# Performance work log

Hardware: AMD Instinct MI355X
Metric: run time of the kernel (lower is better)

Reference implementation:

```python
import jax, jax.numpy as jnp
import numpy as np

N = 200000      # nodes
E = 1600000     # directed edges (before self-loops)
G = 5000        # graphs (molecules)
IN, HID, OUT, HEADS = 128, 128, 128, 3


def gat_layer(x, src, dst, W, a_src, a_dst, b, heads, out_dim, concat):
    n = x.shape[0]
    h = (x @ W).reshape(n, heads, out_dim)                 # [N,H,F]
    al_s = jnp.einsum('nhf,hf->nh', h, a_src)              # [N,H]
    al_d = jnp.einsum('nhf,hf->nh', h, a_dst)
    e = jax.nn.leaky_relu(al_s[src] + al_d[dst], 0.2)      # [E,H]
    m = jax.ops.segment_max(e, dst, num_segments=n)        # softmax over incoming edges
    ex = jnp.exp(e - m[dst])
    den = jax.ops.segment_sum(ex, dst, num_segments=n)
    alpha = ex / (den[dst] + 1e-16)                        # [E,H]
    msg = h[src] * alpha[..., None]                        # [E,H,F]
    agg = jax.ops.segment_sum(msg, dst, num_segments=n)    # [N,H,F]
    agg = agg.reshape(n, heads * out_dim) if concat else agg.mean(axis=1)
    return agg + b


def setup_inputs() -> dict:
    key = jax.random.key(0)
    ks = jax.random.split(key, 16)
    d = {}
    d['x'] = jax.random.normal(ks[0], (N, IN), dtype=jnp.float32)
    d['edge_index'] = jax.random.randint(ks[1], (2, E), 0, N, dtype=jnp.int64)
    d['batch'] = jnp.sort(jax.random.randint(ks[2], (N,), 0, G, dtype=jnp.int64))
    s = 0.1
    d['W1'] = jax.random.normal(ks[3], (IN, HEADS * HID), jnp.float32) * s
    d['a1s'] = jax.random.normal(ks[4], (HEADS, HID), jnp.float32) * s
    d['a1d'] = jax.random.normal(ks[5], (HEADS, HID), jnp.float32) * s
    d['b1'] = jnp.zeros((HEADS * HID,), jnp.float32)
    d['W2'] = jax.random.normal(ks[6], (HEADS * HID, HEADS * HID), jnp.float32) * s
    d['a2s'] = jax.random.normal(ks[7], (HEADS, HID), jnp.float32) * s
    d['a2d'] = jax.random.normal(ks[8], (HEADS, HID), jnp.float32) * s
    d['b2'] = jnp.zeros((HEADS * HID,), jnp.float32)
    d['W3'] = jax.random.normal(ks[9], (HEADS * HID, OUT), jnp.float32) * s
    d['a3s'] = jax.random.normal(ks[10], (1, OUT), jnp.float32) * s
    d['a3d'] = jax.random.normal(ks[11], (1, OUT), jnp.float32) * s
    d['b3'] = jnp.zeros((OUT,), jnp.float32)
    return d


def reference(x, edge_index, batch, W1, a1s, a1d, b1, W2, a2s, a2d, b2, W3, a3s, a3d, b3):
    # PyG GATConv default add_self_loops=True
    loops = jnp.arange(N, dtype=edge_index.dtype)
    src = jnp.concatenate([edge_index[0], loops])
    dst = jnp.concatenate([edge_index[1], loops])
    h = jax.nn.leaky_relu(gat_layer(x, src, dst, W1, a1s, a1d, b1, HEADS, HID, True), 0.2)
    h = jax.nn.leaky_relu(gat_layer(h, src, dst, W2, a2s, a2d, b2, HEADS, HID, True), 0.2)
    h = jax.nn.leaky_relu(gat_layer(h, src, dst, W3, a3s, a3d, b3, 1, OUT, False), 0.2)
    # global mean pool over graphs
    sums = jax.ops.segment_sum(h, batch, num_segments=G)            # [G,OUT]
    cnt = jax.ops.segment_sum(jnp.ones((N,), h.dtype), batch, num_segments=G)
    return sums / jnp.maximum(cnt, 1.0)[:, None]
```

## Files before the change

### kernel.cpp

```cpp
#include <hip/hip_runtime.h>
#include <hip/hip_bf16.h>
#include <math.h>

#define LRELU_SLOPE 0.2f
typedef __hip_bfloat16 bf16;
typedef __hip_bfloat162 bf16x2;

typedef short s8v __attribute__((ext_vector_type(8)));
typedef short s4v __attribute__((ext_vector_type(4)));
typedef float f4v __attribute__((ext_vector_type(4)));
typedef int   i4v __attribute__((ext_vector_type(4)));
typedef unsigned int u4v __attribute__((ext_vector_type(4)));

__device__ __forceinline__ float lrelu(float v) { return v > 0.f ? v : LRELU_SLOPE * v; }
__device__ __forceinline__ float b2f(short b) {
  return __uint_as_float(((unsigned)(unsigned short)b) << 16);
}

__device__ __forceinline__ void st2(float* p, float x, float y) {
  *(float2*)p = float2{x, y};
}

__device__ __forceinline__ u4v make_srd(const void* p) {
  u4v r;
  unsigned long long a = (unsigned long long)p;
  r.x = (unsigned)a; r.y = (unsigned)(a >> 32);
  r.z = 0xFFFFFFFFu;
  r.w = 0x00020000u;
  return r;
}
__device__ __forceinline__ void bstore16_nt(u4v srd, int byteoff, i4v d) {
  asm volatile("buffer_store_dwordx4 %0, %1, %2, 0 offen sc1 nt"
               :: "v"(d), "v"(byteoff), "s"(srd));
}


__global__ void k_zero(unsigned int* __restrict__ p, long n) {
  long i = (long)blockIdx.x * blockDim.x + threadIdx.x;
  if (i < n) p[i] = 0u;
}

__global__ void k_zero_out(float* __restrict__ out, int n) {
  int i = blockIdx.x * blockDim.x + threadIdx.x;
  if (i < n) out[i] = 0.f;
}


__global__ void k_cvt(const float* __restrict__ x, bf16* __restrict__ xb, long n) {
  long i = (long)blockIdx.x * blockDim.x + threadIdx.x;
  if (i < n) xb[i] = __float2bfloat16(x[i]);
}

__global__ void k_tw2(const float* __restrict__ W, bf16* __restrict__ B2, int K, int NN) {
  int tid = blockIdx.x * blockDim.x + threadIdx.x;
  int total = (K * NN) >> 3;
  if (tid >= total) return;
  int f = tid >> 6, l = tid & 63;
  int nfr = NN >> 4;
  int k32 = f / nfr, bnG = f - k32 * nfr;
  int col = bnG * 16 + (l & 15);
  int krow = k32 * 32 + (l >> 4) * 8;
  s8v v;
#pragma unroll
  for (int j = 0; j < 8; ++j) {
    bf16 b = __float2bfloat16(W[(size_t)(krow + j) * NN + col]);
    v[j] = *(short*)&b;
  }
  *(s8v*)&B2[(size_t)tid * 8] = v;
}


__global__ void k_hist(const int* __restrict__ dst, int* __restrict__ deg, int E, int Et) {
  int e = blockIdx.x * blockDim.x + threadIdx.x;
  if (e >= Et) return;
  int d = (e < E) ? dst[e] : (e - E);
  atomicAdd(&deg[d], 1);
}

__global__ void k_hist1(const int* __restrict__ idx, int* __restrict__ deg, int n) {
  int i = blockIdx.x * blockDim.x + threadIdx.x;
  if (i < n) atomicAdd(&deg[idx[i]], 1);
}

__global__ void k_scan1(const int* __restrict__ deg, int* __restrict__ offs,
                        int* __restrict__ bsum, int n) {
  __shared__ int sd[256];
  int t = threadIdx.x;
  int base = blockIdx.x * 1024 + t * 4;
  int v[4]; int tsum = 0;
#pragma unroll
  for (int i = 0; i < 4; ++i) { v[i] = (base + i < n) ? deg[base + i] : 0; tsum += v[i]; }
  sd[t] = tsum;
  __syncthreads();
  for (int off = 1; off < 256; off <<= 1) {
    int x = (t >= off) ? sd[t - off] : 0;
    __syncthreads();
    sd[t] += x;
    __syncthreads();
  }
  int excl = sd[t] - tsum;
#pragma unroll
  for (int i = 0; i < 4; ++i) { if (base + i < n) offs[base + i] = excl; excl += v[i]; }
  if (t == 255) bsum[blockIdx.x] = sd[255];
}

__global__ void k_scan2(int* bsum, int nb) {
  int t = threadIdx.x;
  if (nb > 256) {
    if (t == 0 && blockIdx.x == 0) {
      int run = 0;
      for (int i = 0; i < nb; ++i) { int x = bsum[i]; bsum[i] = run; run += x; }
    }
    return;
  }
  int v = (t < nb) ? bsum[t] : 0;
  int lane = t & 63, wv = t >> 6;
  int s = v;
#pragma unroll
  for (int off = 1; off < 64; off <<= 1) {
    int u = __shfl_up(s, off, 64);
    if (lane >= off) s += u;
  }
  __shared__ int wsum[4];
  if (lane == 63) wsum[wv] = s;
  __syncthreads();
  int add = 0;
  for (int w = 0; w < wv; ++w) add += wsum[w];
  if (t < nb) bsum[t] = add + s - v;
}

__global__ void k_scan3(int* __restrict__ offs, const int* __restrict__ bsum, int n, int total) {
  int t = threadIdx.x;
  int base = blockIdx.x * 1024 + t * 4;
  int add = bsum[blockIdx.x];
#pragma unroll
  for (int i = 0; i < 4; ++i) if (base + i < n) offs[base + i] += add;
  if (blockIdx.x == 0 && t == 0) offs[n] = total;
}

__global__ void k_scatter(const int* __restrict__ src, const int* __restrict__ dst,
                          const int* __restrict__ offs, int* __restrict__ cur,
                          int* __restrict__ ssrc, int E, int Et) {
  int e = blockIdx.x * blockDim.x + threadIdx.x;
  if (e >= Et) return;
  int s, d;
  if (e < E) { s = src[e]; d = dst[e]; } else { s = d = e - E; }
  int pos = offs[d] + atomicAdd(&cur[d], 1);
  ssrc[pos] = s;
}


template <int NT, int K, int NN>
__global__ __launch_bounds__(512) void k_gemm_d(const bf16* __restrict__ A,
                                                const bf16* __restrict__ B2,
                                                bf16* __restrict__ C) {
  constexpr int nk = K >> 5;
  int t = threadIdx.x;
  int wv = t >> 6, lane = t & 63;
  int mg = wv >> 2, ng = wv & 3;
  int quad = lane >> 4, l15 = lane & 15;
  size_t bm0 = (size_t)blockIdx.x * 64;
  const bf16* Ap0 = A + (bm0 + mg * 32 + l15) * (size_t)K + quad * 8;
  const bf16* Ap1 = Ap0 + (size_t)16 * K;
  constexpr int nfr = NN >> 4;
  const bf16* Bp = B2 + ((size_t)(ng * NT) << 9) + lane * 8;
  constexpr size_t fstep = (size_t)nfr << 9;

  f4v acc[2][NT];
#pragma unroll
  for (int ms = 0; ms < 2; ++ms)
#pragma unroll
    for (int bn = 0; bn < NT; ++bn) acc[ms][bn] = f4v{0, 0, 0, 0};

  s8v pa0[3], pa1[3], pb[3][NT];
#define GLOAD(ik, sl)                                                        \
  do {                                                                       \
    pa0[sl] = *(const s8v*)(Ap0 + (ik) * 32);                                \
    pa1[sl] = *(const s8v*)(Ap1 + (ik) * 32);                                \
    _Pragma("unroll")                                                        \
    for (int bn = 0; bn < NT; ++bn)                                          \
      pb[sl][bn] = *(const s8v*)(Bp + (ik) * fstep + bn * 512);              \
  } while (0)

  GLOAD(0, 0);
  if constexpr (nk > 1) GLOAD(1, 1);
  if constexpr (nk > 2) GLOAD(2, 2);

#pragma unroll
  for (int ik = 0; ik < nk; ++ik) {
    const int c = ik % 3;
#pragma unroll
    for (int bn = 0; bn < NT; ++bn)
      acc[0][bn] = __builtin_amdgcn_mfma_f32_16x16x32_bf16(pa0[c], pb[c][bn], acc[0][bn], 0, 0, 0);
#pragma unroll
    for (int bn = 0; bn < NT; ++bn)
      acc[1][bn] = __builtin_amdgcn_mfma_f32_16x16x32_bf16(pa1[c], pb[c][bn], acc[1][bn], 0, 0, 0);
    if (ik + 3 < nk) GLOAD(ik + 3, c);
  }
#undef GLOAD

#pragma unroll
  for (int ms = 0; ms < 2; ++ms)
#pragma unroll
    for (int bn = 0; bn < NT; ++bn) {
      int coln = (ng * NT + bn) * 16 + l15;
      size_t rbase = bm0 + mg * 32 + ms * 16 + quad * 4;
#pragma unroll
      for (int r = 0; r < 4; ++r)
        C[(rbase + r) * NN + coln] = __float2bfloat16(acc[ms][bn][r]);
    }
}


template <int H>
__global__ void k_al(const bf16* __restrict__ h, const float* __restrict__ as,
                     const float* __restrict__ ad, float* __restrict__ al_s,
                     float* __restrict__ al_d, int N) {
  constexpr int SP = (H > 1) ? 4 : 1;
  int n = (blockIdx.x * blockDim.x + threadIdx.x) >> 6;
  int lane = threadIdx.x & 63;
  if (n >= N) return;
  int hd = lane >> 4;
  bool active = (hd < H);
  int hdc = active ? hd : 0;
  int f8 = (lane & 15) * 8;
  const bf16* hp = h + (size_t)n * (H * 128) + hdc * 128 + f8;
  s8v hv = *(const s8v*)hp;
  float ss = 0.f, sd = 0.f;
#pragma unroll
  for (int i = 0; i < 8; ++i) {
    float v = b2f(hv[i]);
    ss += v * as[hdc * 128 + f8 + i];
    sd += v * ad[hdc * 128 + f8 + i];
  }
#pragma unroll
  for (int off = 8; off; off >>= 1) {
    ss += __shfl_xor(ss, off, 64);
    sd += __shfl_xor(sd, off, 64);
  }
  if (active && (lane & 15) == 0) {
    al_s[n * SP + hd] = ss;
    al_d[n * SP + hd] = sd;
  }
}


template <int CPL> struct HVec;
template <> struct HVec<8> { typedef s8v T; };
template <> struct HVec<4> { typedef s4v T; };

template <int H, typename OT>
__global__ __launch_bounds__(256) void k_attn_agg(const bf16* __restrict__ hbuf,
                           const int* __restrict__ ssrc,
                           const int* __restrict__ offs, const float* __restrict__ al_s,
                           const float* __restrict__ al_d, const float* __restrict__ bias,
                           OT* __restrict__ out, int N) {
  constexpr int SW  = (H > 1) ? 4 : 2;
  constexpr int ROW = H * 128;
  constexpr int CPL = (H > 1) ? 8 : 4;
  constexpr int NL  = ROW / CPL;
  typedef typename HVec<CPL>::T hvec;

  __shared__ __align__(16) float stash[4][64 * SW];
  int n = (blockIdx.x * blockDim.x + threadIdx.x) >> 6;
  int lane = threadIdx.x & 63;
  if (n >= N) return;
  float* st = stash[threadIdx.x >> 6];
  int start = offs[n], end = offs[n + 1];

  float ald[H];
  if constexpr (H > 1) {
    float4 t = *(const float4*)&al_d[(size_t)n * 4];
    ald[0] = t.x; ald[1] = t.y; ald[2] = t.z;
  } else {
    ald[0] = al_d[n];
  }

  bool act = lane < NL;
  int c0 = act ? lane * CPL : 0;
  int hd_l = c0 >> 7;

  float m[H];
  float den = 0.f;
  float acc[CPL];
#pragma unroll
  for (int hd = 0; hd < H; ++hd) m[hd] = -1e30f;
#pragma unroll
  for (int i = 0; i < CPL; ++i) acc[i] = 0.f;

  for (int cb = start; cb < end; cb += 64) {
    int cl = end - cb; if (cl > 64) cl = 64;
    bool el = lane < cl;
    int mys = el ? ssrc[cb + lane] : 0;
    float ev[H];
    if constexpr (H > 1) {
      float4 av = *(const float4*)&al_s[(size_t)mys * 4];
      ev[0] = av.x; ev[1] = av.y; ev[2] = av.z;
    } else {
      ev[0] = al_s[mys];
    }
#pragma unroll
    for (int hd = 0; hd < H; ++hd)
      ev[hd] = el ? lrelu(ev[hd] + ald[hd]) : -1e30f;

    float nm[H];
#pragma unroll
    for (int hd = 0; hd < H; ++hd) {
      float v = ev[hd];
#pragma unroll
      for (int off = 32; off; off >>= 1) v = fmaxf(v, __shfl_xor(v, off, 64));
      nm[hd] = fmaxf(v, m[hd]);
    }
    if (cb > start) {
      float sc[H];
#pragma unroll
      for (int hd = 0; hd < H; ++hd) sc[hd] = __expf(m[hd] - nm[hd]);
      float so = sc[hd_l];
      den *= so;
#pragma unroll
      for (int i = 0; i < CPL; ++i) acc[i] *= so;
    }
#pragma unroll
    for (int hd = 0; hd < H; ++hd) m[hd] = nm[hd];

    float myex[H];
#pragma unroll
    for (int hd = 0; hd < H; ++hd) myex[hd] = el ? __expf(ev[hd] - m[hd]) : 0.f;

    __builtin_amdgcn_wave_barrier();
    if constexpr (H > 1) {
      float4 s4{__int_as_float(mys), myex[0], myex[1], myex[2]};
      *(float4*)&st[lane * 4] = s4;
    } else {
      float2 s2{__int_as_float(mys), myex[0]};
      *(float2*)&st[lane * 2] = s2;
    }
    asm volatile("s_waitcnt lgkmcnt(0)" ::: "memory");
    __builtin_amdgcn_wave_barrier();

    for (int r = 0; r < cl; r += 8) {
      int su[8]; float a[8];
#pragma unroll
      for (int u = 0; u < 8; ++u) {
        if constexpr (H > 1) {
          float4 ed = *(const float4*)&st[(r + u) * 4];
          su[u] = __float_as_int(ed.x);
          a[u] = (hd_l == 0) ? ed.y : ((hd_l == 1) ? ed.z : ed.w);
        } else {
          float2 ed = *(const float2*)&st[(r + u) * 2];
          su[u] = __float_as_int(ed.x);
          a[u] = ed.y;
        }
        den += a[u];
      }
      hvec hv[8];
#pragma unroll
      for (int u = 0; u < 8; ++u)
        hv[u] = *(const hvec*)(hbuf + (size_t)su[u] * ROW + c0);
#pragma unroll
      for (int u = 0; u < 8; ++u)
#pragma unroll
        for (int i = 0; i < CPL; ++i)
          acc[i] += a[u] * b2f(hv[u][i]);
    }
  }

  if (act) {
    float rr = 1.f / (den + 1e-16f);
    u4v srd = make_srd(out);
    int boff = (int)(((size_t)n * ROW + c0) * sizeof(OT));
    if constexpr (sizeof(OT) == 2) {
      union { s8v s; i4v i; } u;
#pragma unroll
      for (int i = 0; i < CPL; ++i) {
        float o = lrelu(acc[i] * rr + bias[c0 + i]);
        bf16 b = __float2bfloat16(o);
        u.s[i] = *(short*)&b;
      }
      bstore16_nt(srd, boff, u.i);
    } else {
      union { float4 f; i4v i; } u;
      u.f.x = lrelu(acc[0] * rr + bias[c0 + 0]);
      u.f.y = lrelu(acc[1] * rr + bias[c0 + 1]);
      u.f.z = lrelu(acc[2] * rr + bias[c0 + 2]);
      u.f.w = lrelu(acc[3] * rr + bias[c0 + 3]);
      bstore16_nt(srd, boff, u.i);
    }
  }
}


__global__ void k_pool(const float* __restrict__ h, const int* __restrict__ goffs,
                       float* __restrict__ out, int G) {
  int g = (blockIdx.x * blockDim.x + threadIdx.x) >> 6;
  int lane = threadIdx.x & 63;
  if (g >= G) return;
  int s = goffs[g], e = goffs[g + 1];
  float ax = 0.f, ay = 0.f;
  for (int n = s; n < e; ++n) {
    float2 v = *(const float2*)&h[(size_t)n * 128 + lane * 2];
    ax += v.x; ay += v.y;
  }
  float c = fmaxf((float)(e - s), 1.f);
  st2(&out[(size_t)g * 128 + lane * 2], ax / c, ay / c);
}


extern "C" void kernel_launch(void* const* d_in, const int* in_sizes, int n_in,
                              void* d_out, int out_size, void* d_ws, size_t ws_size,
                              hipStream_t stream) {
  const float* x   = (const float*)d_in[0];
  const int*   ei  = (const int*)d_in[1];
  const int*   bat = (const int*)d_in[2];
  const float* W1  = (const float*)d_in[3];
  const float* a1s = (const float*)d_in[4];
  const float* a1d = (const float*)d_in[5];
  const float* b1  = (const float*)d_in[6];
  const float* W2  = (const float*)d_in[7];
  const float* a2s = (const float*)d_in[8];
  const float* a2d = (const float*)d_in[9];
  const float* b2  = (const float*)d_in[10];
  const float* W3  = (const float*)d_in[11];
  const float* a3s = (const float*)d_in[12];
  const float* a3d = (const float*)d_in[13];
  const float* b3  = (const float*)d_in[14];
  float* out = (float*)d_out;

  const int N = in_sizes[2];
  const int E = in_sizes[1] / 2;
  const int Et = E + N;
  const int G = out_size / 128;

  char* p = (char*)d_ws;
  auto carve = [&](size_t bytes) { void* r = (void*)p; p += (bytes + 255) & ~(size_t)255; return r; };
  bf16*  bufA   = (bf16*)carve((size_t)N * 384 * 2);
  bf16*  bufB   = (bf16*)carve((size_t)N * 384 * 2);
  float* al_s   = (float*)carve((size_t)N * 4 * 4);
  float* al_d   = (float*)carve((size_t)N * 4 * 4);
  int*   ssrc   = (int*)carve((size_t)Et * 4);
  int*   offs   = (int*)carve((size_t)(N + 1) * 4);
  int*   deg    = (int*)carve((size_t)N * 4);
  int*   cur    = (int*)carve((size_t)N * 4);
  int*   bsum   = (int*)carve(4096 * 4);
  int*   gdeg   = (int*)carve((size_t)G * 4);
  int*   goffs  = (int*)carve((size_t)(G + 1) * 4);
  bf16*  Wp1    = (bf16*)carve((size_t)384 * 128 * 2);
  bf16*  Wp2    = (bf16*)carve((size_t)384 * 384 * 2);
  bf16*  Wp3    = (bf16*)carve((size_t)128 * 384 * 2);
  size_t need = (size_t)(p - (char*)d_ws);

  if (ws_size < need) {
    k_zero_out<<<(out_size + 255) / 256, 256, 0, stream>>>(out, out_size);
    return;
  }

  const int* esrc = ei;
  const int* edst = ei + E;

  int ebl = (Et + 255) / 256;
  int NB = (N + 1023) / 1024;
  int GB = (G + 1023) / 1024;
  int nodeWaveBlocks = (N * 64 + 255) / 256;
  int gemmBlocks = (N + 63) / 64;

  bf16* xb = bufA;
  k_cvt<<<((long)N * 128 + 255) / 256, 256, 0, stream>>>(x, xb, (long)N * 128);
  k_tw2<<<(128 * 384 / 8 + 255) / 256, 256, 0, stream>>>(W1, Wp1, 128, 384);
  k_tw2<<<(384 * 384 / 8 + 255) / 256, 256, 0, stream>>>(W2, Wp2, 384, 384);
  k_tw2<<<(384 * 128 / 8 + 255) / 256, 256, 0, stream>>>(W3, Wp3, 384, 128);

  k_zero<<<(N + 255) / 256, 256, 0, stream>>>((unsigned int*)deg, N);
  k_hist<<<ebl, 256, 0, stream>>>(edst, deg, E, Et);
  k_scan1<<<NB, 256, 0, stream>>>(deg, offs, bsum, N);
  k_scan2<<<1, 256, 0, stream>>>(bsum, NB);
  k_scan3<<<NB, 256, 0, stream>>>(offs, bsum, N, Et);
  k_zero<<<(N + 255) / 256, 256, 0, stream>>>((unsigned int*)cur, N);
  k_scatter<<<ebl, 256, 0, stream>>>(esrc, edst, offs, cur, ssrc, E, Et);

  k_zero<<<(G + 255) / 256, 256, 0, stream>>>((unsigned int*)gdeg, G);
  k_hist1<<<(N + 255) / 256, 256, 0, stream>>>(bat, gdeg, N);
  k_scan1<<<GB, 256, 0, stream>>>(gdeg, goffs, bsum, G);
  k_scan2<<<1, 256, 0, stream>>>(bsum, GB);
  k_scan3<<<GB, 256, 0, stream>>>(goffs, bsum, G, N);

  k_gemm_d<6, 128, 384><<<gemmBlocks, 512, 0, stream>>>(xb, Wp1, bufB);
  k_al<3><<<nodeWaveBlocks, 256, 0, stream>>>(bufB, a1s, a1d, al_s, al_d, N);
  k_attn_agg<3, bf16><<<nodeWaveBlocks, 256, 0, stream>>>(bufB, ssrc, offs, al_s, al_d, b1, bufA, N);

  k_gemm_d<6, 384, 384><<<gemmBlocks, 512, 0, stream>>>(bufA, Wp2, bufB);
  k_al<3><<<nodeWaveBlocks, 256, 0, stream>>>(bufB, a2s, a2d, al_s, al_d, N);
  k_attn_agg<3, bf16><<<nodeWaveBlocks, 256, 0, stream>>>(bufB, ssrc, offs, al_s, al_d, b2, bufA, N);

  k_gemm_d<2, 384, 128><<<gemmBlocks, 512, 0, stream>>>(bufA, Wp3, bufB);
  k_al<1><<<nodeWaveBlocks, 256, 0, stream>>>(bufB, a3s, a3d, al_s, al_d, N);
  float* out3 = (float*)bufA;
  k_attn_agg<1, float><<<nodeWaveBlocks, 256, 0, stream>>>(bufB, ssrc, offs, al_s, al_d, b3, out3, N);

  k_pool<<<(G * 64 + 255) / 256, 256, 0, stream>>>(out3, goffs, out, G);
}
```

Before: 1.503 ms.

## Tile node GEMMs 256x128 with async LDS staging of A

Replaces the register-prefetch 64-row GEMM with a 256-row by 128-column tiled kernel. The A tile is staged into swizzled, double-buffered LDS through global_load_lds, while B fragments are read straight from global memory. Each wave now computes a 4x4 grid of MFMA tiles, which raises data reuse and cuts redundant A reads across column tiles. The intermediate buffers are padded to a multiple of 256 rows so the last tile can read and write past N. The cost is a block-wide barrier on every k-step and heavier LDS and register use.

```diff
diff --git a/kernel.cpp b/kernel.cpp
--- a/kernel.cpp
+++ b/kernel.cpp
@@ -57,8 +57,8 @@
   if (tid >= total) return;
   int f = tid >> 6, l = tid & 63;
   int nfr = NN >> 4;
-  int k32 = f / nfr, bnG = f - k32 * nfr;
-  int col = bnG * 16 + (l & 15);
+  int k32 = f / nfr, ct = f - k32 * nfr;
+  int col = ct * 16 + (l & 15);
   int krow = k32 * 32 + (l >> 4) * 8;
   s8v v;
 #pragma unroll
@@ -150,61 +150,79 @@
 }
 
 
-template <int NT, int K, int NN>
-__global__ __launch_bounds__(512) void k_gemm_d(const bf16* __restrict__ A,
-                                                const bf16* __restrict__ B2,
-                                                bf16* __restrict__ C) {
-  constexpr int nk = K >> 5;
+template <int K, int NN>
+__global__ __launch_bounds__(512, 4) void k_gemm_t(const bf16* __restrict__ A,
+                                                   const bf16* __restrict__ B2,
+                                                   bf16* __restrict__ C) {
+  constexpr int nk = K / 32;
+  constexpr int nfr = NN >> 4;
+  __shared__ __align__(16) short sA[2][256 * 32];
   int t = threadIdx.x;
   int wv = t >> 6, lane = t & 63;
-  int mg = wv >> 2, ng = wv & 3;
+  int mg = wv >> 1, ng = wv & 1;
   int quad = lane >> 4, l15 = lane & 15;
-  size_t bm0 = (size_t)blockIdx.x * 64;
-  const bf16* Ap0 = A + (bm0 + mg * 32 + l15) * (size_t)K + quad * 8;
-  const bf16* Ap1 = Ap0 + (size_t)16 * K;
-  constexpr int nfr = NN >> 4;
-  const bf16* Bp = B2 + ((size_t)(ng * NT) << 9) + lane * 8;
-  constexpr size_t fstep = (size_t)nfr << 9;
-
-  f4v acc[2][NT];
-#pragma unroll
-  for (int ms = 0; ms < 2; ++ms)
-#pragma unroll
-    for (int bn = 0; bn < NT; ++bn) acc[ms][bn] = f4v{0, 0, 0, 0};
-
-  s8v pa0[3], pa1[3], pb[3][NT];
-#define GLOAD(ik, sl)                                                        \
-  do {                                                                       \
-    pa0[sl] = *(const s8v*)(Ap0 + (ik) * 32);                                \
-    pa1[sl] = *(const s8v*)(Ap1 + (ik) * 32);                                \
-    _Pragma("unroll")                                                        \
-    for (int bn = 0; bn < NT; ++bn)                                          \
-      pb[sl][bn] = *(const s8v*)(Bp + (ik) * fstep + bn * 512);              \
+  size_t bm0 = (size_t)blockIdx.x * 256;
+  int ctb = blockIdx.y * 8 + ng * 4;
+
+  int sr = t >> 2, p = t & 3;
+  int c = p ^ (sr & 3);
+  const bf16* g0 = A + (bm0 + sr) * (size_t)K + c * 8;
+  const bf16* g1 = g0 + (size_t)128 * K;
+  const bf16* Bp = B2 + ((size_t)ctb << 9) + lane * 8;
+
+  f4v acc[4][4];
+#pragma unroll
+  for (int ms = 0; ms < 4; ++ms)
+#pragma unroll
+    for (int bn = 0; bn < 4; ++bn) acc[ms][bn] = f4v{0, 0, 0, 0};
+
+#define STAGE(step, buf)                                                        \
+  do {                                                                          \
+    __builtin_amdgcn_global_load_lds(                                           \
+        (const __attribute__((address_space(1))) void*)(g0 + (step) * 32),      \
+        (__attribute__((address_space(3))) void*)((char*)sA[buf] + wv * 1024),  \
+        16, 0, 0);                                                              \
+    __builtin_amdgcn_global_load_lds(                                           \
+        (const __attribute__((address_space(1))) void*)(g1 + (step) * 32),      \
+        (__attribute__((address_space(3))) void*)((char*)sA[buf] + 8192 + wv * 1024), \
+        16, 0, 0);                                                              \
   } while (0)
 
-  GLOAD(0, 0);
-  if constexpr (nk > 1) GLOAD(1, 1);
-  if constexpr (nk > 2) GLOAD(2, 2);
-
-#pragma unroll
+  STAGE(0, 0);
+  __syncthreads();
+
   for (int ik = 0; ik < nk; ++ik) {
-    const int c = ik % 3;
-#pragma unroll
-    for (int bn = 0; bn < NT; ++bn)
-      acc[0][bn] = __builtin_amdgcn_mfma_f32_16x16x32_bf16(pa0[c], pb[c][bn], acc[0][bn], 0, 0, 0);
-#pragma unroll
-    for (int bn = 0; bn < NT; ++bn)
-      acc[1][bn] = __builtin_amdgcn_mfma_f32_16x16x32_bf16(pa1[c], pb[c][bn], acc[1][bn], 0, 0, 0);
-    if (ik + 3 < nk) GLOAD(ik + 3, c);
-  }
-#undef GLOAD
-
-#pragma unroll
-  for (int ms = 0; ms < 2; ++ms)
-#pragma unroll
-    for (int bn = 0; bn < NT; ++bn) {
-      int coln = (ng * NT + bn) * 16 + l15;
-      size_t rbase = bm0 + mg * 32 + ms * 16 + quad * 4;
+    int cur = ik & 1;
+    if (ik + 1 < nk) STAGE(ik + 1, cur ^ 1);
+
+    const char* sb = (const char*)sA[cur];
+    s8v af[4];
+#pragma unroll
+    for (int ms = 0; ms < 4; ++ms) {
+      int row = mg * 64 + ms * 16 + l15;
+      int pos = quad ^ (row & 3);
+      af[ms] = *(const s8v*)(sb + row * 64 + pos * 16);
+    }
+    s8v pb[4];
+#pragma unroll
+    for (int bn = 0; bn < 4; ++bn)
+      pb[bn] = *(const s8v*)(Bp + ((size_t)(ik * nfr + bn) << 9));
+#pragma unroll
+    for (int ms = 0; ms < 4; ++ms)
+#pragma unroll
+      for (int bn = 0; bn < 4; ++bn)
+        acc[ms][bn] = __builtin_amdgcn_mfma_f32_16x16x32_bf16(af[ms], pb[bn], acc[ms][bn], 0, 0, 0);
+
+    __syncthreads();
+  }
+#undef STAGE
+
+#pragma unroll
+  for (int ms = 0; ms < 4; ++ms)
+#pragma unroll
+    for (int bn = 0; bn < 4; ++bn) {
+      int coln = (ctb + bn) * 16 + l15;
+      size_t rbase = bm0 + mg * 64 + ms * 16 + quad * 4;
 #pragma unroll
       for (int r = 0; r < 4; ++r)
         C[(rbase + r) * NN + coln] = __float2bfloat16(acc[ms][bn][r]);
@@ -431,10 +449,13 @@
   const int Et = E + N;
   const int G = out_size / 128;
 
+  const int MB = (N + 255) / 256;
+  const int Mpad = MB * 256;
+
   char* p = (char*)d_ws;
   auto carve = [&](size_t bytes) { void* r = (void*)p; p += (bytes + 255) & ~(size_t)255; return r; };
-  bf16*  bufA   = (bf16*)carve((size_t)N * 384 * 2);
-  bf16*  bufB   = (bf16*)carve((size_t)N * 384 * 2);
+  bf16*  bufA   = (bf16*)carve((size_t)Mpad * 384 * 2);
+  bf16*  bufB   = (bf16*)carve((size_t)Mpad * 384 * 2);
   float* al_s   = (float*)carve((size_t)N * 4 * 4);
   float* al_d   = (float*)carve((size_t)N * 4 * 4);
   int*   ssrc   = (int*)carve((size_t)Et * 4);
@@ -461,7 +482,6 @@
   int NB = (N + 1023) / 1024;
   int GB = (G + 1023) / 1024;
   int nodeWaveBlocks = (N * 64 + 255) / 256;
-  int gemmBlocks = (N + 63) / 64;
 
   bf16* xb = bufA;
   k_cvt<<<((long)N * 128 + 255) / 256, 256, 0, stream>>>(x, xb, (long)N * 128);
@@ -483,15 +503,15 @@
   k_scan2<<<1, 256, 0, stream>>>(bsum, GB);
   k_scan3<<<GB, 256, 0, stream>>>(goffs, bsum, G, N);
 
-  k_gemm_d<6, 128, 384><<<gemmBlocks, 512, 0, stream>>>(xb, Wp1, bufB);
+  k_gemm_t<128, 384><<<dim3(MB, 3), 512, 0, stream>>>(xb, Wp1, bufB);
   k_al<3><<<nodeWaveBlocks, 256, 0, stream>>>(bufB, a1s, a1d, al_s, al_d, N);
   k_attn_agg<3, bf16><<<nodeWaveBlocks, 256, 0, stream>>>(bufB, ssrc, offs, al_s, al_d, b1, bufA, N);
 
-  k_gemm_d<6, 384, 384><<<gemmBlocks, 512, 0, stream>>>(bufA, Wp2, bufB);
+  k_gemm_t<384, 384><<<dim3(MB, 3), 512, 0, stream>>>(bufA, Wp2, bufB);
   k_al<3><<<nodeWaveBlocks, 256, 0, stream>>>(bufB, a2s, a2d, al_s, al_d, N);
   k_attn_agg<3, bf16><<<nodeWaveBlocks, 256, 0, stream>>>(bufB, ssrc, offs, al_s, al_d, b2, bufA, N);
 
-  k_gemm_d<2, 384, 128><<<gemmBlocks, 512, 0, stream>>>(bufA, Wp3, bufB);
+  k_gemm_t<384, 128><<<dim3(MB, 1), 512, 0, stream>>>(bufA, Wp3, bufB);
   k_al<1><<<nodeWaveBlocks, 256, 0, stream>>>(bufB, a3s, a3d, al_s, al_d, N);
   float* out3 = (float*)bufA;
   k_attn_agg<1, float><<<nodeWaveBlocks, 256, 0, stream>>>(bufB, ssrc, offs, al_s, al_d, b3, out3, N);
```

After: 1.399 ms. -6.9%, faster.
